# Performance work log

Hardware: AMD Instinct MI355X
Metric: run time of the kernel (lower is better)

## Reference

```python
import jax, jax.numpy as jnp
import numpy as np

DIM = 256
HEADS = 8
RES = (8, 60, 120)
WIN = (2, 6, 12)
HID = 4 * DIM
EPS = 1e-5


def get_earth_position_index(window_size):
    wpl, wlat, wlon = window_size
    zi = np.arange(wpl)
    zj = -np.arange(wpl) * wpl
    hi = np.arange(wlat)
    hj = -np.arange(wlat) * wlat
    w = np.arange(wlon)
    c1 = np.stack(np.meshgrid(zi, hi, w, indexing='ij')).reshape(3, -1)
    c2 = np.stack(np.meshgrid(zj, hj, w, indexing='ij')).reshape(3, -1)
    coords = (c1[:, :, None] - c2[:, None, :]).transpose(1, 2, 0)
    coords[:, :, 2] += wlon - 1
    coords[:, :, 1] *= 2 * wlon - 1
    coords[:, :, 0] *= (2 * wlon - 1) * wlat * wlat
    return coords.sum(-1)  # [N, N] int indices into bias table rows


POS_IDX = get_earth_position_index(WIN)


def layernorm(x, g, b):
    mu = x.mean(-1, keepdims=True)
    var = ((x - mu) ** 2).mean(-1, keepdims=True)
    return (x - mu) * jax.lax.rsqrt(var + EPS) * g + b


def setup_inputs() -> dict:
    key = jax.random.key(0)
    ks = jax.random.split(key, 8)
    Pl, Lat, Lon = RES
    B = 2
    L = Pl * Lat * Lon
    tow = (Pl // WIN[0]) * (Lat // WIN[1])            # type_of_windows = 40
    tbl = WIN[0] ** 2 * WIN[1] ** 2 * (2 * WIN[2] - 1)  # 3312 bias rows
    s = lambda k, shp: jax.random.normal(k, shp, jnp.float32) * 0.02
    return {
        'x': jax.random.normal(ks[0], (B, L, DIM), jnp.float32),
        'norm1_g': jnp.ones((DIM,), jnp.float32),
        'norm1_b': jnp.zeros((DIM,), jnp.float32),
        'qkv_w': s(ks[1], (3 * DIM, DIM)),
        'qkv_b': jnp.zeros((3 * DIM,), jnp.float32),
        'bias_table': s(ks[2], (tbl, tow, HEADS)),
        'proj_w': s(ks[3], (DIM, DIM)),
        'proj_b': jnp.zeros((DIM,), jnp.float32),
        'norm2_g': jnp.ones((DIM,), jnp.float32),
        'norm2_b': jnp.zeros((DIM,), jnp.float32),
        'fc1_w': s(ks[4], (HID, DIM)),
        'fc1_b': jnp.zeros((HID,), jnp.float32),
        'fc2_w': s(ks[5], (DIM, HID)),
        'fc2_b': jnp.zeros((DIM,), jnp.float32),
    }


def reference(x, norm1_g, norm1_b, qkv_w, qkv_b, bias_table, proj_w, proj_b,
              norm2_g, norm2_b, fc1_w, fc1_b, fc2_w, fc2_b):
    Pl, Lat, Lon = RES
    wpl, wlat, wlon = WIN
    B, L, C = x.shape
    H = HEADS
    hd = C // H
    nPl, nLat, nLon = Pl // wpl, Lat // wlat, Lon // wlon

    shortcut = x
    h = layernorm(x, norm1_g, norm1_b).reshape(B, Pl, Lat, Lon, C)

    # window_partition: -> [B*nLon, nPl*nLat, N, C]  (roll_type=0 -> no roll, no mask)
    h = h.reshape(B, nPl, wpl, nLat, wlat, nLon, wlon, C)
    win = h.transpose(0, 5, 1, 3, 2, 4, 6, 7).reshape(
        B * nLon, nPl * nLat, wpl * wlat * wlon, C)
    B_, nW, N, _ = win.shape

    # EarthAttention3D
    qkv = jnp.einsum('bwnc,dc->bwnd', win, qkv_w) + qkv_b
    qkv = qkv.reshape(B_, nW, N, 3, H, hd).transpose(3, 0, 4, 1, 2, 5)
    q = qkv[0] * (hd ** -0.5)        # [B_, H, nW, N, hd]
    k, v = qkv[1], qkv[2]
    attn = jnp.einsum('bhwnd,bhwmd->bhwnm', q, k)
    # gathered earth position bias: [H, nW, N, N]
    bias = bias_table[POS_IDX.reshape(-1)].reshape(N, N, nW, H).transpose(3, 2, 0, 1)
    attn = jax.nn.softmax(attn + bias[None], axis=-1)
    out = jnp.einsum('bhwnm,bhwmd->bhwnd', attn, v)
    out = out.transpose(0, 2, 3, 1, 4).reshape(B_, nW, N, C)
    out = jnp.einsum('bwnc,dc->bwnd', out, proj_w) + proj_b

    # window_reverse: -> [B, Pl, Lat, Lon, C]
    out = out.reshape(B, nLon, nPl, nLat, wpl, wlat, wlon, C)
    out = out.transpose(0, 2, 4, 3, 5, 1, 6, 7).reshape(B, Pl, Lat, Lon, C)
    h = out.reshape(B, L, C)

    x = shortcut + h  # dt=1, drop_path=Identity
    m = layernorm(x, norm2_g, norm2_b)
    m = jax.nn.gelu(jnp.einsum('blc,hc->blh', m, fc1_w) + fc1_b, approximate=False)
    m = jnp.einsum('blh,ch->blc', m, fc2_w) + fc2_b
    return x + m
```

## Files before the change

### kernel.cpp

```cpp
#include <hip/hip_runtime.h>
#include <cstdint>
#include <cstddef>


typedef __attribute__((ext_vector_type(8))) short bf16x8;
typedef __attribute__((ext_vector_type(4))) float f32x4;
typedef unsigned short ushort_t;

#define MFMA16(a, b, c) __builtin_amdgcn_mfma_f32_16x16x32_bf16(a, b, c, 0, 0, 0)

__device__ __forceinline__ unsigned short f2bf(float f) {
  union { float f; unsigned u; } c; c.f = f;
  unsigned r = c.u + 0x7FFFu + ((c.u >> 16) & 1u);
  return (unsigned short)(r >> 16);
}

__device__ __forceinline__ void gload16(const void* g, void* l) {
  __builtin_amdgcn_global_load_lds(
      (const __attribute__((address_space(1))) unsigned int*)g,
      (__attribute__((address_space(3))) unsigned int*)(uintptr_t)l,
      16, 0, 0);
}

__global__ void cvt_kernel(const float* __restrict__ in, ushort_t* __restrict__ out, int n) {
  int i = blockIdx.x * 256 + threadIdx.x;
  if (i < n) out[i] = f2bf(in[i]);
}

__global__ void tbl_transpose(const float* __restrict__ tbl, float* __restrict__ out) {
  const int i = blockIdx.x * 256 + threadIdx.x;
  if (i < 320 * 3312) {
    const int wh = i / 3312, idx = i % 3312;
    out[i] = tbl[idx * 320 + wh];
  }
}

__global__ __launch_bounds__(256) void ln_kernel(
    const float* __restrict__ in, const float* __restrict__ g,
    const float* __restrict__ b, ushort_t* __restrict__ out) {
  const int wid = threadIdx.x >> 6, lane = threadIdx.x & 63;
  const size_t tok = (size_t)blockIdx.x * 4 + wid;
  const float4 v = *(const float4*)(in + tok * 256 + lane * 4);
  float s  = v.x + v.y + v.z + v.w;
  float sq = v.x * v.x + v.y * v.y + v.z * v.z + v.w * v.w;
#pragma unroll
  for (int off = 1; off < 64; off <<= 1) {
    s  += __shfl_xor(s, off);
    sq += __shfl_xor(sq, off);
  }
  const float mu = s * (1.0f / 256.0f);
  const float rs = rsqrtf(sq * (1.0f / 256.0f) - mu * mu + 1e-5f);
  const float4 gg = *(const float4*)(g + lane * 4);
  const float4 bb = *(const float4*)(b + lane * 4);
  ushort4 st;
  st.x = f2bf((v.x - mu) * rs * gg.x + bb.x);
  st.y = f2bf((v.y - mu) * rs * gg.y + bb.y);
  st.z = f2bf((v.z - mu) * rs * gg.z + bb.z);
  st.w = f2bf((v.w - mu) * rs * gg.w + bb.w);
  *(ushort4*)(out + tok * 256 + lane * 4) = st;
}

template <int EPI>
__global__ __launch_bounds__(256) void gemm_kernel(
    const ushort_t* __restrict__ A, const ushort_t* __restrict__ Bw,
    const float* __restrict__ bias, const float* __restrict__ res,
    void* __restrict__ outp, int M, int N, int K) {
  __shared__ unsigned char lds[32768];
  unsigned char* ldsA = lds;
  unsigned char* ldsB = lds + 16384;
  const int tid = threadIdx.x;
  const int lane = tid & 63, wid = tid >> 6;
  const int ntn = N >> 7;
  const int tileM = (int)(blockIdx.x / ntn) << 7;
  const int tileN = (int)(blockIdx.x % ntn) << 7;
  const unsigned baseoff = ((unsigned)wid << 10) | ((unsigned)lane << 4);

  f32x4 acc[4][4];
#pragma unroll
  for (int i = 0; i < 4; i++)
#pragma unroll
    for (int j = 0; j < 4; j++) acc[i][j] = (f32x4){0.f, 0.f, 0.f, 0.f};

  const int wm = (wid >> 1) << 6;
  const int wn = (wid & 1) << 6;

  for (int k0 = 0; k0 < K; k0 += 64) {
#pragma unroll
    for (int i = 0; i < 4; i++) {
      const unsigned o = baseoff + (unsigned)i * 4096u;
      const unsigned row = o >> 7, cb = o & 127u;
      const unsigned scb = cb ^ ((row & 7u) << 4);
      gload16(A + (size_t)(tileM + row) * K + k0 + (scb >> 1),
              ldsA + (i << 12) + (wid << 10));
      gload16(Bw + (size_t)(tileN + row) * K + k0 + (scb >> 1),
              ldsB + (i << 12) + (wid << 10));
    }
    asm volatile("s_waitcnt vmcnt(0)" ::: "memory");
    __syncthreads();
#pragma unroll
    for (int ks = 0; ks < 2; ks++) {
      bf16x8 af[4], bf[4];
#pragma unroll
      for (int mi = 0; mi < 4; mi++) {
        const int row = wm + mi * 16 + (lane & 15);
        const unsigned cb = ((unsigned)(ks * 64) + (((unsigned)lane >> 4) << 4)) ^ ((row & 7) << 4);
        af[mi] = *(const bf16x8*)(ldsA + row * 128 + cb);
      }
#pragma unroll
      for (int ni = 0; ni < 4; ni++) {
        const int row = wn + ni * 16 + (lane & 15);
        const unsigned cb = ((unsigned)(ks * 64) + (((unsigned)lane >> 4) << 4)) ^ ((row & 7) << 4);
        bf[ni] = *(const bf16x8*)(ldsB + row * 128 + cb);
      }
#pragma unroll
      for (int mi = 0; mi < 4; mi++)
#pragma unroll
        for (int ni = 0; ni < 4; ni++)
          acc[mi][ni] = MFMA16(af[mi], bf[ni], acc[mi][ni]);
    }
    __syncthreads();
  }

  const int cr = ((lane >> 4) << 2);
  const int cc = lane & 15;
#pragma unroll
  for (int mi = 0; mi < 4; mi++) {
#pragma unroll
    for (int ni = 0; ni < 4; ni++) {
      const int colg = tileN + wn + ni * 16 + cc;
      const float bv = bias[colg];
#pragma unroll
      for (int r = 0; r < 4; r++) {
        const int rowg = tileM + wm + mi * 16 + cr + r;
        const size_t oidx = (size_t)rowg * N + colg;
        float v = acc[mi][ni][r] + bv;
        if (EPI == 0) {
          if (colg < 256) v *= 0.17677669529663687f;
          ((ushort_t*)outp)[oidx] = f2bf(v);
        } else if (EPI == 1) {
          ((float*)outp)[oidx] = v + res[oidx];
        } else if (EPI == 2) {
          const float ge = 0.5f * v * (1.0f + erff(v * 0.7071067811865475f));
          ((ushort_t*)outp)[oidx] = f2bf(ge);
        } else {
          ((float*)outp)[oidx] = v + res[oidx];
        }
      }
    }
  }
}

__device__ __forceinline__ int Lidx3(int n, int pi, int li, int ln) {
  const int wp = n / 72, rem = n - wp * 72;
  const int wl = rem / 12, ww = rem - wl * 12;
  return ((pi * 2 + wp) * 60 + li * 6 + wl) * 120 + ln * 12 + ww;
}

__global__ __launch_bounds__(256) void attn_kernel(
    const ushort_t* __restrict__ qkv,
    const float* __restrict__ tblT,
    ushort_t* __restrict__ outp) {
  __shared__ float    tslice[3312];
  __shared__ ushort_t Vt[32 * 168];
  __shared__ ushort_t Pw[4][16 * 168];

  const int bi = blockIdx.x;
  const int h  = bi & 7;
  const int w  = (bi >> 3) % 40;
  const int b_ = bi / 320;
  const int b  = b_ / 10, ln = b_ % 10;
  const int pi = w / 10,  li = w % 10;
  const int tid = threadIdx.x, lane = tid & 63, wid = tid >> 6;
  const int lr = lane & 15, hi = lane >> 4;
  const size_t tokbase = (size_t)b * 57600;

  const float* tsl = tblT + (size_t)(w * 8 + h) * 3312;
  for (int i = tid; i < 3312; i += 256) tslice[i] = tsl[i];

  for (int idx = tid; idx < 160 * 32; idx += 256) {
    const int n = idx >> 5, e = idx & 31;
    ushort_t val = 0;
    if (n < 144) {
      const size_t rb = (tokbase + Lidx3(n, pi, li, ln)) * 768 + 512 + h * 32 + e;
      val = qkv[rb];
    }
    Vt[e * 168 + n] = val;
  }
  __syncthreads();

  for (int fr = wid; fr < 9; fr += 4) {
    const int qn = fr * 16 + lr;
    const bf16x8 qf = *(const bf16x8*)(
        qkv + (tokbase + Lidx3(qn, pi, li, ln)) * 768 + h * 32 + hi * 8);

    f32x4 s[9];
#pragma unroll
    for (int fc = 0; fc < 9; fc++) {
      const int kn = fc * 16 + lr;
      const bf16x8 kf = *(const bf16x8*)(
          qkv + (tokbase + Lidx3(kn, pi, li, ln)) * 768 + 256 + h * 32 + hi * 8);
      f32x4 z = (f32x4){0.f, 0.f, 0.f, 0.f};
      s[fc] = MFMA16(qf, kf, z);
    }

    int aoff[4];
#pragma unroll
    for (int r = 0; r < 4; r++) {
      const int n = fr * 16 + hi * 4 + r;
      const int zq = n / 72, hq = (n / 12) % 6, wq = n % 12;
      aoff[r] = zq * 828 + hq * 23 + wq + 11;
    }
#pragma unroll
    for (int fc = 0; fc < 9; fc++) {
      const int m = fc * 16 + lr;
      const int zk = m / 72, hk = (m / 12) % 6, wk = m % 12;
      const int boff = zk * 1656 + hk * 138 - wk;
#pragma unroll
      for (int r = 0; r < 4; r++)
        s[fc][r] += tslice[aoff[r] + boff];
    }

    float mx[4], sm[4];
#pragma unroll
    for (int r = 0; r < 4; r++) mx[r] = -1e30f;
#pragma unroll
    for (int fc = 0; fc < 9; fc++)
#pragma unroll
      for (int r = 0; r < 4; r++) mx[r] = fmaxf(mx[r], s[fc][r]);
#pragma unroll
    for (int off = 1; off < 16; off <<= 1)
#pragma unroll
      for (int r = 0; r < 4; r++) mx[r] = fmaxf(mx[r], __shfl_xor(mx[r], off));
#pragma unroll
    for (int r = 0; r < 4; r++) sm[r] = 0.f;
#pragma unroll
    for (int fc = 0; fc < 9; fc++)
#pragma unroll
      for (int r = 0; r < 4; r++) {
        s[fc][r] = __expf(s[fc][r] - mx[r]);
        sm[r] += s[fc][r];
      }
#pragma unroll
    for (int off = 1; off < 16; off <<= 1)
#pragma unroll
      for (int r = 0; r < 4; r++) sm[r] += __shfl_xor(sm[r], off);
    float inv[4];
#pragma unroll
    for (int r = 0; r < 4; r++) inv[r] = 1.0f / sm[r];

    ushort_t* pw = Pw[wid];
#pragma unroll
    for (int fc = 0; fc < 9; fc++)
#pragma unroll
      for (int r = 0; r < 4; r++)
        pw[(hi * 4 + r) * 168 + fc * 16 + lr] = f2bf(s[fc][r] * inv[r]);
#pragma unroll
    for (int r = 0; r < 4; r++)
      pw[(hi * 4 + r) * 168 + 144 + lr] = 0;

#pragma unroll
    for (int fcv = 0; fcv < 2; fcv++) {
      f32x4 acc = (f32x4){0.f, 0.f, 0.f, 0.f};
#pragma unroll
      for (int kb = 0; kb < 5; kb++) {
        const bf16x8 a  = *(const bf16x8*)(pw + lr * 168 + kb * 32 + hi * 8);
        const bf16x8 bb = *(const bf16x8*)(Vt + (fcv * 16 + lr) * 168 + kb * 32 + hi * 8);
        acc = MFMA16(a, bb, acc);
      }
      const int e = fcv * 16 + lr;
#pragma unroll
      for (int r = 0; r < 4; r++) {
        const int n = fr * 16 + hi * 4 + r;
        const size_t ob = (tokbase + Lidx3(n, pi, li, ln)) * 256 + h * 32 + e;
        outp[ob] = f2bf(acc[r]);
      }
    }
  }
}

extern "C" void kernel_launch(void* const* d_in, const int* in_sizes, int n_in,
                              void* d_out, int out_size, void* d_ws, size_t ws_size,
                              hipStream_t stream) {
  const float* x      = (const float*)d_in[0];
  const float* n1g    = (const float*)d_in[1];
  const float* n1b    = (const float*)d_in[2];
  const float* qkv_w  = (const float*)d_in[3];
  const float* qkv_b  = (const float*)d_in[4];
  const float* btab   = (const float*)d_in[5];
  const float* proj_w = (const float*)d_in[6];
  const float* proj_b = (const float*)d_in[7];
  const float* n2g    = (const float*)d_in[8];
  const float* n2b    = (const float*)d_in[9];
  const float* fc1_w  = (const float*)d_in[10];
  const float* fc1_b  = (const float*)d_in[11];
  const float* fc2_w  = (const float*)d_in[12];
  const float* fc2_b  = (const float*)d_in[13];
  float* outp = (float*)d_out;

  char* ws = (char*)d_ws;
  ushort_t* qkvbuf = (ushort_t*)(ws);
  ushort_t* hbuf   = (ushort_t*)(ws + 176947200);
  float*    tblT   = (float*)(ws + 235929600);
  ushort_t* ln2buf = (ushort_t*)(ws);
  ushort_t* fc1buf = (ushort_t*)(ws + 58982400);
  ushort_t* wbuf   = (ushort_t*)(ws + 294912000);
  ushort_t* qkvW = wbuf;
  ushort_t* projW = wbuf + 196608;
  ushort_t* fc1W  = wbuf + 262144;
  ushort_t* fc2W  = wbuf + 524288;

  cvt_kernel<<<768,  256, 0, stream>>>(qkv_w,  qkvW, 196608);
  cvt_kernel<<<256,  256, 0, stream>>>(proj_w, projW, 65536);
  cvt_kernel<<<1024, 256, 0, stream>>>(fc1_w,  fc1W, 262144);
  cvt_kernel<<<1024, 256, 0, stream>>>(fc2_w,  fc2W, 262144);

  ln_kernel<<<28800, 256, 0, stream>>>(x, n1g, n1b, hbuf);
  tbl_transpose<<<4140, 256, 0, stream>>>(btab, tblT);

  gemm_kernel<0><<<900 * 6, 256, 0, stream>>>(hbuf, qkvW, qkv_b, nullptr, qkvbuf, 115200, 768, 256);
  attn_kernel<<<6400, 256, 0, stream>>>(qkvbuf, tblT, hbuf);
  gemm_kernel<1><<<900 * 2, 256, 0, stream>>>(hbuf, projW, proj_b, x, outp, 115200, 256, 256);
  ln_kernel<<<28800, 256, 0, stream>>>(outp, n2g, n2b, ln2buf);
  gemm_kernel<2><<<900 * 8, 256, 0, stream>>>(ln2buf, fc1W, fc1_b, nullptr, fc1buf, 115200, 1024, 256);
  gemm_kernel<3><<<900 * 2, 256, 0, stream>>>(fc1buf, fc2W, fc2_b, outp, outp, 115200, 256, 1024);
}
```

Measured before the change: 936.2 us.

## Store QKV in window-major order and precompute dense attention bias

The QKV GEMM epilogue now scatters rows through a token-to-window permutation, so attention reads each window's tokens contiguously. The proj GEMM gathers rows back to natural order through the inverse permutation. Attention now reads a precomputed dense per-(head, window) bias array instead of staging a table slice in LDS, runs 192-thread blocks with vectorized output stores, and both GEMM and attention remap block indices across XCDs. This adds a large bias-gather pass and permutation setup each call, and the bias reads move from LDS to global memory.

```diff
diff --git a/kernel.cpp b/kernel.cpp
--- a/kernel.cpp
+++ b/kernel.cpp
@@ -22,17 +22,38 @@
       16, 0, 0);
 }
 
-__global__ void cvt_kernel(const float* __restrict__ in, ushort_t* __restrict__ out, int n) {
-  int i = blockIdx.x * 256 + threadIdx.x;
-  if (i < n) out[i] = f2bf(in[i]);
-}
-
-__global__ void tbl_transpose(const float* __restrict__ tbl, float* __restrict__ out) {
+__global__ void cvt_all(const float* __restrict__ a, const float* __restrict__ b,
+                        const float* __restrict__ c, const float* __restrict__ d,
+                        ushort_t* __restrict__ out) {
   const int i = blockIdx.x * 256 + threadIdx.x;
-  if (i < 320 * 3312) {
-    const int wh = i / 3312, idx = i % 3312;
-    out[i] = tbl[idx * 320 + wh];
-  }
+  float v;
+  if (i < 196608) v = a[i];
+  else if (i < 262144) v = b[i - 196608];
+  else if (i < 524288) v = c[i - 262144];
+  else v = d[i - 524288];
+  out[i] = f2bf(v);
+}
+
+__global__ void make_perm(int* __restrict__ w2n, int* __restrict__ n2w) {
+  const int wr = blockIdx.x * 256 + threadIdx.x;
+  const int n = wr % 144, w = (wr / 144) % 40, b_ = wr / 5760;
+  const int b = b_ / 10, ln = b_ % 10, pi = w / 10, li = w % 10;
+  const int wp = n / 72, rem = n % 72, wl = rem / 12, ww = rem % 12;
+  const int nat = b * 57600 + ((pi * 2 + wp) * 60 + li * 6 + wl) * 120 + ln * 12 + ww;
+  w2n[wr] = nat;
+  n2w[nat] = wr;
+}
+
+__global__ void bias_gather(const float* __restrict__ tbl, float* __restrict__ out) {
+  const int t = blockIdx.x * 256 + threadIdx.x;
+  const int m = t % 144;
+  const int n = (t / 144) % 144;
+  const int wh = t / 20736;
+  const int w = wh % 40, h = wh / 40;
+  const int zq = n / 72, hq = (n / 12) % 6, wq = n % 12;
+  const int zk = m / 72, hk = (m / 12) % 6, wk = m % 12;
+  const int idx = (zq + 2 * zk) * 828 + (hq + 6 * hk) * 23 + (wq - wk + 11);
+  out[t] = tbl[idx * 320 + w * 8 + h];
 }
 
 __global__ __launch_bounds__(256) void ln_kernel(
@@ -64,15 +85,18 @@
 __global__ __launch_bounds__(256) void gemm_kernel(
     const ushort_t* __restrict__ A, const ushort_t* __restrict__ Bw,
     const float* __restrict__ bias, const float* __restrict__ res,
-    void* __restrict__ outp, int M, int N, int K) {
+    const int* __restrict__ perm, void* __restrict__ outp,
+    int M, int N, int K) {
   __shared__ unsigned char lds[32768];
   unsigned char* ldsA = lds;
   unsigned char* ldsB = lds + 16384;
   const int tid = threadIdx.x;
   const int lane = tid & 63, wid = tid >> 6;
   const int ntn = N >> 7;
-  const int tileM = (int)(blockIdx.x / ntn) << 7;
-  const int tileN = (int)(blockIdx.x % ntn) << 7;
+  const int cpx = (int)gridDim.x >> 3;
+  const int orig = ((int)blockIdx.x & 7) * cpx + ((int)blockIdx.x >> 3);
+  const int tileM = (orig / ntn) << 7;
+  const int tileN = (orig % ntn) << 7;
   const unsigned baseoff = ((unsigned)wid << 10) | ((unsigned)lane << 4);
 
   f32x4 acc[4][4];
@@ -125,14 +149,19 @@
   const int cc = lane & 15;
 #pragma unroll
   for (int mi = 0; mi < 4; mi++) {
+    int srow[4];
+#pragma unroll
+    for (int r = 0; r < 4; r++) {
+      const int rowg = tileM + wm + mi * 16 + cr + r;
+      srow[r] = (EPI <= 1) ? perm[rowg] : rowg;
+    }
 #pragma unroll
     for (int ni = 0; ni < 4; ni++) {
       const int colg = tileN + wn + ni * 16 + cc;
       const float bv = bias[colg];
 #pragma unroll
       for (int r = 0; r < 4; r++) {
-        const int rowg = tileM + wm + mi * 16 + cr + r;
-        const size_t oidx = (size_t)rowg * N + colg;
+        const size_t oidx = (size_t)srow[r] * N + colg;
         float v = acc[mi][ni][r] + bv;
         if (EPI == 0) {
           if (colg < 256) v *= 0.17677669529663687f;
@@ -150,75 +179,57 @@
   }
 }
 
-__device__ __forceinline__ int Lidx3(int n, int pi, int li, int ln) {
-  const int wp = n / 72, rem = n - wp * 72;
-  const int wl = rem / 12, ww = rem - wl * 12;
-  return ((pi * 2 + wp) * 60 + li * 6 + wl) * 120 + ln * 12 + ww;
-}
-
-__global__ __launch_bounds__(256) void attn_kernel(
+__global__ __launch_bounds__(192, 4) void attn_kernel(
     const ushort_t* __restrict__ qkv,
-    const float* __restrict__ tblT,
+    const float* __restrict__ biasArr,
     ushort_t* __restrict__ outp) {
-  __shared__ float    tslice[3312];
-  __shared__ ushort_t Vt[32 * 168];
-  __shared__ ushort_t Pw[4][16 * 168];
+  __shared__ ushort_t Vt[32 * 184];
+  __shared__ ushort_t Pw[3][16 * 184];
 
   const int bi = blockIdx.x;
-  const int h  = bi & 7;
-  const int w  = (bi >> 3) % 40;
-  const int b_ = bi / 320;
-  const int b  = b_ / 10, ln = b_ % 10;
-  const int pi = w / 10,  li = w % 10;
-  const int tid = threadIdx.x, lane = tid & 63, wid = tid >> 6;
+  const int orig = (bi & 7) * 800 + (bi >> 3);
+  const int h  = orig & 7;
+  const int wg = orig >> 3;
+  const int w  = wg % 40;
+  const int tid = threadIdx.x, lane = tid & 63, wid = tid / 64;
   const int lr = lane & 15, hi = lane >> 4;
-  const size_t tokbase = (size_t)b * 57600;
-
-  const float* tsl = tblT + (size_t)(w * 8 + h) * 3312;
-  for (int i = tid; i < 3312; i += 256) tslice[i] = tsl[i];
-
-  for (int idx = tid; idx < 160 * 32; idx += 256) {
+  const size_t wbase = (size_t)wg * 144;
+  const ushort_t* qbase = qkv + wbase * 768 + h * 32;
+
+  for (int idx = tid; idx < 4608; idx += 192) {
     const int n = idx >> 5, e = idx & 31;
-    ushort_t val = 0;
-    if (n < 144) {
-      const size_t rb = (tokbase + Lidx3(n, pi, li, ln)) * 768 + 512 + h * 32 + e;
-      val = qkv[rb];
-    }
-    Vt[e * 168 + n] = val;
+    Vt[e * 184 + n] = qbase[(size_t)n * 768 + 512 + e];
+  }
+  for (int idx = tid; idx < 512; idx += 192)
+    Vt[(idx >> 4) * 184 + 144 + (idx & 15)] = 0;
+  {
+    ushort_t* pw = Pw[wid];
+#pragma unroll
+    for (int r = 0; r < 4; r++) pw[(hi * 4 + r) * 184 + 144 + lr] = 0;
   }
   __syncthreads();
 
-  for (int fr = wid; fr < 9; fr += 4) {
-    const int qn = fr * 16 + lr;
-    const bf16x8 qf = *(const bf16x8*)(
-        qkv + (tokbase + Lidx3(qn, pi, li, ln)) * 768 + h * 32 + hi * 8);
+  const float* bb0 = biasArr + (size_t)(h * 40 + w) * 20736;
+  ushort_t* pw = Pw[wid];
+
+  for (int it = 0; it < 3; it++) {
+    const int fr = wid * 3 + it;
+    const bf16x8 qf = *(const bf16x8*)(qbase + (size_t)(fr * 16 + lr) * 768 + hi * 8);
 
     f32x4 s[9];
 #pragma unroll
     for (int fc = 0; fc < 9; fc++) {
-      const int kn = fc * 16 + lr;
-      const bf16x8 kf = *(const bf16x8*)(
-          qkv + (tokbase + Lidx3(kn, pi, li, ln)) * 768 + 256 + h * 32 + hi * 8);
+      const bf16x8 kf = *(const bf16x8*)(qbase + (size_t)(fc * 16 + lr) * 768 + 256 + hi * 8);
       f32x4 z = (f32x4){0.f, 0.f, 0.f, 0.f};
       s[fc] = MFMA16(qf, kf, z);
     }
 
-    int aoff[4];
-#pragma unroll
-    for (int r = 0; r < 4; r++) {
-      const int n = fr * 16 + hi * 4 + r;
-      const int zq = n / 72, hq = (n / 12) % 6, wq = n % 12;
-      aoff[r] = zq * 828 + hq * 23 + wq + 11;
-    }
-#pragma unroll
-    for (int fc = 0; fc < 9; fc++) {
-      const int m = fc * 16 + lr;
-      const int zk = m / 72, hk = (m / 12) % 6, wk = m % 12;
-      const int boff = zk * 1656 + hk * 138 - wk;
+    const float* brow = bb0 + (size_t)(fr * 16 + hi * 4) * 144 + lr;
+#pragma unroll
+    for (int fc = 0; fc < 9; fc++)
 #pragma unroll
       for (int r = 0; r < 4; r++)
-        s[fc][r] += tslice[aoff[r] + boff];
-    }
+        s[fc][r] += brow[(size_t)r * 144 + fc * 16];
 
     float mx[4], sm[4];
 #pragma unroll
@@ -248,32 +259,25 @@
 #pragma unroll
     for (int r = 0; r < 4; r++) inv[r] = 1.0f / sm[r];
 
-    ushort_t* pw = Pw[wid];
 #pragma unroll
     for (int fc = 0; fc < 9; fc++)
 #pragma unroll
       for (int r = 0; r < 4; r++)
-        pw[(hi * 4 + r) * 168 + fc * 16 + lr] = f2bf(s[fc][r] * inv[r]);
-#pragma unroll
-    for (int r = 0; r < 4; r++)
-      pw[(hi * 4 + r) * 168 + 144 + lr] = 0;
-
-#pragma unroll
-    for (int fcv = 0; fcv < 2; fcv++) {
+        pw[(hi * 4 + r) * 184 + fc * 16 + lr] = f2bf(s[fc][r] * inv[r]);
+
+#pragma unroll
+    for (int eblk = 0; eblk < 2; eblk++) {
       f32x4 acc = (f32x4){0.f, 0.f, 0.f, 0.f};
 #pragma unroll
       for (int kb = 0; kb < 5; kb++) {
-        const bf16x8 a  = *(const bf16x8*)(pw + lr * 168 + kb * 32 + hi * 8);
-        const bf16x8 bb = *(const bf16x8*)(Vt + (fcv * 16 + lr) * 168 + kb * 32 + hi * 8);
+        const bf16x8 a  = *(const bf16x8*)(Vt + (eblk * 16 + lr) * 184 + kb * 32 + hi * 8);
+        const bf16x8 bb = *(const bf16x8*)(pw + lr * 184 + kb * 32 + hi * 8);
         acc = MFMA16(a, bb, acc);
       }
-      const int e = fcv * 16 + lr;
-#pragma unroll
-      for (int r = 0; r < 4; r++) {
-        const int n = fr * 16 + hi * 4 + r;
-        const size_t ob = (tokbase + Lidx3(n, pi, li, ln)) * 256 + h * 32 + e;
-        outp[ob] = f2bf(acc[r]);
-      }
+      ushort4 st;
+      st.x = f2bf(acc[0]); st.y = f2bf(acc[1]);
+      st.z = f2bf(acc[2]); st.w = f2bf(acc[3]);
+      *(ushort4*)(outp + (wbase + fr * 16 + lr) * 256 + h * 32 + eblk * 16 + hi * 4) = st;
     }
   }
 }
@@ -300,7 +304,9 @@
   char* ws = (char*)d_ws;
   ushort_t* qkvbuf = (ushort_t*)(ws);
   ushort_t* hbuf   = (ushort_t*)(ws + 176947200);
-  float*    tblT   = (float*)(ws + 235929600);
+  float*    biasA  = (float*)(ws + 235929600);
+  int*      n2w    = (int*)(ws + 262471680);
+  int*      w2n    = (int*)(ws + 262932480);
   ushort_t* ln2buf = (ushort_t*)(ws);
   ushort_t* fc1buf = (ushort_t*)(ws + 58982400);
   ushort_t* wbuf   = (ushort_t*)(ws + 294912000);
@@ -309,18 +315,15 @@
   ushort_t* fc1W  = wbuf + 262144;
   ushort_t* fc2W  = wbuf + 524288;
 
-  cvt_kernel<<<768,  256, 0, stream>>>(qkv_w,  qkvW, 196608);
-  cvt_kernel<<<256,  256, 0, stream>>>(proj_w, projW, 65536);
-  cvt_kernel<<<1024, 256, 0, stream>>>(fc1_w,  fc1W, 262144);
-  cvt_kernel<<<1024, 256, 0, stream>>>(fc2_w,  fc2W, 262144);
-
+  cvt_all<<<3072, 256, 0, stream>>>(qkv_w, proj_w, fc1_w, fc2_w, wbuf);
+  make_perm<<<450, 256, 0, stream>>>(w2n, n2w);
+  bias_gather<<<25920, 256, 0, stream>>>(btab, biasA);
   ln_kernel<<<28800, 256, 0, stream>>>(x, n1g, n1b, hbuf);
-  tbl_transpose<<<4140, 256, 0, stream>>>(btab, tblT);
-
-  gemm_kernel<0><<<900 * 6, 256, 0, stream>>>(hbuf, qkvW, qkv_b, nullptr, qkvbuf, 115200, 768, 256);
-  attn_kernel<<<6400, 256, 0, stream>>>(qkvbuf, tblT, hbuf);
-  gemm_kernel<1><<<900 * 2, 256, 0, stream>>>(hbuf, projW, proj_b, x, outp, 115200, 256, 256);
+
+  gemm_kernel<0><<<5400, 256, 0, stream>>>(hbuf, qkvW, qkv_b, nullptr, n2w, qkvbuf, 115200, 768, 256);
+  attn_kernel<<<6400, 192, 0, stream>>>(qkvbuf, biasA, hbuf);
+  gemm_kernel<1><<<1800, 256, 0, stream>>>(hbuf, projW, proj_b, x, w2n, outp, 115200, 256, 256);
   ln_kernel<<<28800, 256, 0, stream>>>(outp, n2g, n2b, ln2buf);
-  gemm_kernel<2><<<900 * 8, 256, 0, stream>>>(ln2buf, fc1W, fc1_b, nullptr, fc1buf, 115200, 1024, 256);
-  gemm_kernel<3><<<900 * 2, 256, 0, stream>>>(fc1buf, fc2W, fc2_b, outp, outp, 115200, 256, 1024);
-}
+  gemm_kernel<2><<<7200, 256, 0, stream>>>(ln2buf, fc1W, fc1_b, nullptr, nullptr, fc1buf, 115200, 1024, 256);
+  gemm_kernel<3><<<1800, 256, 0, stream>>>(fc1buf, fc2W, fc2_b, outp, nullptr, outp, 115200, 256, 1024);
+}
```

Result: slower. 1.079 ms (+15.2%).
